# Optimization experiments

Measured on AMD Instinct MI355X. Metric: run time of the kernel, lower is better.

The kernel has to match this reference:

```python
import jax, jax.numpy as jnp
import numpy as np

N, F, E = 1024, 32, 20


def setup_inputs() -> dict:
    key = jax.random.key(0)
    ks = jax.random.split(key, 18)
    f32 = jnp.float32
    nrm = lambda k, shape, s=1.0: (jax.random.normal(k, shape, f32) * s)
    scalar = nrm(ks[0], (N, 1, F))
    vector = nrm(ks[1], (N, 3, F))
    expansion = nrm(ks[2], (N, N, E))
    d = nrm(ks[3], (N, N, 3))
    direction = d / (jnp.linalg.norm(d, axis=-1, keepdims=True) + 1e-6)
    mask = (jax.random.uniform(ks[4], (N, N, 1)) < 0.9).astype(f32)
    w = 0.1  # weight scale
    return {
        "scalar": scalar, "vector": vector, "expansion": expansion,
        "direction": direction, "mask": mask,
        # message.msg_left: Linear(F,F) -> SiLU -> Linear(F,3F)
        "mL_w1": nrm(ks[5], (F, F), w), "mL_b1": jnp.zeros((F,), f32),
        "mL_w2": nrm(ks[6], (F, 3 * F), w), "mL_b2": jnp.zeros((3 * F,), f32),
        # message.msg_right: Linear(E, 3F)
        "mR_w": nrm(ks[7], (E, 3 * F), w), "mR_b": jnp.zeros((3 * F,), f32),
        # update.upd_right: Linear(2F,F) -> SiLU -> Linear(F,3F)
        "uR_w1": nrm(ks[8], (2 * F, F), w), "uR_b1": jnp.zeros((F,), f32),
        "uR_w2": nrm(ks[9], (F, 3 * F), w), "uR_b2": jnp.zeros((3 * F,), f32),
        # update.U / update.V: Linear(F,F,bias=False)
        "U_w": nrm(ks[10], (F, F), w),
        "V_w": nrm(ks[11], (F, F), w),
    }


def _message(s, v, expansion, direction, mask,
             mL_w1, mL_b1, mL_w2, mL_b2, mR_w, mR_b):
    # msg_left(s): [N,1,F] -> [N,1,3F]
    left = jax.nn.silu(s @ mL_w1 + mL_b1) @ mL_w2 + mL_b2
    # msg_right(expansion): [N,N,E] -> [N,N,3F] -> [N,N,1,3F]
    right = (expansion @ mR_w + mR_b)[..., None, :]
    prod = left * right                      # [N,N,1,3F]
    a, b, c = jnp.split(prod, 3, axis=-1)    # each [N,N,1,F]
    mask_ = mask[..., None]                  # [N,N,1,1]
    delta_s = jnp.sum(mask_ * b, axis=-3)    # [N,1,F]
    dv = v * a + direction[..., None] * c    # [N,N,3,F]
    delta_v = jnp.sum(mask_ * dv, axis=-3)   # [N,3,F]
    return delta_s, delta_v


def _update(scalar, vector, uR_w1, uR_b1, uR_w2, uR_b2, U_w, V_w):
    left = vector @ U_w                      # [N,3,F]
    right = vector @ V_w                     # [N,3,F]
    right_norm = jnp.linalg.norm(right, axis=-2, keepdims=True)   # [N,1,F]
    feats = jnp.concatenate((scalar, right_norm), axis=-1)        # [N,1,2F]
    feats = jax.nn.silu(feats @ uR_w1 + uR_b1) @ uR_w2 + uR_b2    # [N,1,3F]
    a, b, c = jnp.split(feats, 3, axis=-1)
    delta_v = a * left                                            # [N,3,F]
    inner = jnp.sum(left * right, axis=-2, keepdims=True)         # [N,1,F]
    delta_s = inner * b + c
    return delta_s, delta_v


def reference(scalar, vector, expansion, direction, mask,
              mL_w1, mL_b1, mL_w2, mL_b2, mR_w, mR_b,
              uR_w1, uR_b1, uR_w2, uR_b2, U_w, V_w):
    ds, dv = _message(scalar, vector, expansion, direction, mask,
                      mL_w1, mL_b1, mL_w2, mL_b2, mR_w, mR_b)
    scalar = scalar + ds
    vector = vector + dv
    ds, dv = _update(scalar, vector, uR_w1, uR_b1, uR_w2, uR_b2, U_w, V_w)
    return scalar + ds, vector + dv
```

## Files before the change

### kernel.cpp

```cpp
#include <hip/hip_runtime.h>
#include <hip/hip_bf16.h>
#include <math.h>

#define NN 1024
#define JS 512
#define NSL 2
#define LP 40

typedef __attribute__((ext_vector_type(8))) short v8s;
typedef __attribute__((ext_vector_type(4))) float v4f;

#define MFMA(a, b, c) __builtin_amdgcn_mfma_f32_16x16x32_bf16((a), (b), (c), 0, 0, 0)

#define BAR() asm volatile("s_waitcnt lgkmcnt(0)\n\ts_barrier" ::: "memory")
#define VM0() asm volatile("s_waitcnt vmcnt(0)" ::: "memory")

static __device__ __forceinline__ void gll16(const void* g, void* l) {
    __builtin_amdgcn_global_load_lds(
        (const __attribute__((address_space(1))) unsigned int*)g,
        (__attribute__((address_space(3))) unsigned int*)l, 16, 0, 0);
}

static __device__ __forceinline__ float silu_f(float x) {
    return x / (1.0f + __expf(-x));
}
static __device__ __forceinline__ unsigned short f2bf(float x) {
    __hip_bfloat16 h = __float2bfloat16(x);
    unsigned short u; __builtin_memcpy(&u, &h, 2); return u;
}
static __device__ __forceinline__ unsigned pack2bf(float lo, float hi) {
    __hip_bfloat162 h = __float22bfloat162_rn(make_float2(lo, hi));
    unsigned u; __builtin_memcpy(&u, &h, 4); return u;
}

extern "C" __global__ __launch_bounds__(128)
void node_kernel(const float* __restrict__ scalar,
                 const float* __restrict__ vector,
                 const float* __restrict__ mL_w1, const float* __restrict__ mL_b1,
                 const float* __restrict__ mL_w2, const float* __restrict__ mL_b2,
                 unsigned short* __restrict__ RT)
{
    const int j = blockIdx.x;
    const int t = threadIdx.x;
    __shared__ float ss[32], sh[32], sleft[96];

    if (t < 32) ss[t] = scalar[j * 32 + t];
    __syncthreads();
    if (t < 32) {
        float a = mL_b1[t];
        #pragma unroll
        for (int k = 0; k < 32; k++) a = fmaf(ss[k], mL_w1[k * 32 + t], a);
        sh[t] = silu_f(a);
    }
    __syncthreads();
    if (t < 96) {
        float a = mL_b2[t];
        #pragma unroll
        for (int k = 0; k < 32; k++) a = fmaf(sh[k], mL_w2[k * 96 + t], a);
        sleft[t] = a;
    }
    __syncthreads();
    for (int n = t; n < 160; n += 128) {
        float val;
        if (n < 32)        val = sleft[32 + n];
        else if (n < 128)  val = vector[j * 96 + (n - 32)] * sleft[(n - 32) & 31];
        else               val = sleft[64 + (n - 128)];
        const int jsw = j ^ ((n & 7) << 3);
        RT[(size_t)n * NN + jsw] = f2bf(val);
    }
}

extern "C" __global__ __launch_bounds__(256, 4)
void edge_mfma_kernel(const float* __restrict__ expansion,
                      const float* __restrict__ direction,
                      const float* __restrict__ mask,
                      const float* __restrict__ mR_w, const float* __restrict__ mR_b,
                      const unsigned short* __restrict__ RT,
                      float* __restrict__ part)
{
    const int t = threadIdx.x;
    const int wave = t >> 6;
    const int lane = t & 63;
    const int lrow = lane & 15;
    const int quad = lane >> 4;
    const int jp = lane >> 2;
    const int g  = lane & 3;
    const int jl = jp * 2;

    const int bx = blockIdx.x;
    const int slice = bx & (NSL - 1);
    const int j0 = slice * JS;
    const int iw = wave >> 1;
    const int i = (bx >> 1) * 2 + iw;

    __shared__ __align__(16) unsigned short BSm[160 * 64];
    __shared__ __align__(16) char Wm[13824];
    __shared__ __align__(16) float mLds[2 * JS];

    const unsigned short* rtbase = RT + ((size_t)(t >> 3) * NN) + ((t & 7) * 8) + j0;
    unsigned short* lds_dst = BSm + t * 8;

    #pragma unroll
    for (int k = 0; k < 5; ++k)
        gll16(rtbase + (size_t)k * 32 * NN, lds_dst + k * 2048);
    for (int q = t; q < 2 * JS; q += 256)
        mLds[q] = mask[(size_t)((bx >> 1) * 2 + (q >> 9)) * NN + j0 + (q & 511)];
    VM0();
    BAR();

    const int kswz = (lrow & 7) << 3;
    const int ko = quad * 8;

    if ((wave & 1) == 0) {
        unsigned short* L1 = (unsigned short*)(Wm + iw * 6912);
        float* S = (float*)((char*)BSm + iw * 5472);

        v4f acc[16];
        #pragma unroll
        for (int q = 0; q < 16; ++q) acc[q] = (v4f){0.f, 0.f, 0.f, 0.f};

        const float* expA = expansion + ((size_t)i * NN + j0 + jl) * 20;

        float4 fa = *(const float4*)(expA + 4 * g);
        float4 fb = *(const float4*)(expA + 20 + 4 * g);
        float cea = expA[16 + g], ceb = expA[36 + g];
        float2 mc = *(const float2*)(&mLds[iw * JS + jl]);

        for (int ss2 = 0; ss2 < 8; ++ss2) {
            #pragma unroll
            for (int ch = 0; ch < 2; ++ch) {
                {
                    const float ea[4] = {fa.x, fa.y, fa.z, fa.w};
                    const float eb[4] = {fb.x, fb.y, fb.z, fb.w};
                    #pragma unroll
                    for (int k = 0; k < 4; ++k)
                        *(unsigned*)(L1 + (4 * g + k) * LP + jl) =
                            pack2bf(mc.x * ea[k], mc.y * eb[k]);
                    *(unsigned*)(L1 + (16 + g) * LP + jl) = pack2bf(mc.x * cea, mc.y * ceb);
                    if (g == 0) *(unsigned*)(L1 + 20 * LP + jl) = pack2bf(mc.x, mc.y);
                }
                {
                    const int u = ss2 * 2 + ch;
                    const int un = (u < 15) ? u + 1 : 15;
                    fa = *(const float4*)(expA + un * 640 + 4 * g);
                    fb = *(const float4*)(expA + un * 640 + 20 + 4 * g);
                    cea = expA[un * 640 + 16 + g];
                    ceb = expA[un * 640 + 36 + g];
                    mc = *(const float2*)(&mLds[iw * JS + un * 32 + jl]);
                }
                {
                    const v8s a0 = *(const v8s*)(L1 + lrow * LP + ko);
                    const v8s a1 = *(const v8s*)(L1 + (16 + lrow) * LP + ko);
                    const int klz = (ch * 32 + ko) ^ kswz;
                    #pragma unroll
                    for (int nt = 0; nt < 8; ++nt) {
                        const v8s b = *(const v8s*)(BSm + (nt * 16 + lrow) * 64 + klz);
                        acc[nt]     = MFMA(a0, b, acc[nt]);
                        acc[8 + nt] = MFMA(a1, b, acc[8 + nt]);
                    }
                }
            }
            BAR();
            if (ss2 < 7) {
                const unsigned short* src = rtbase + (ss2 + 1) * 64;
                #pragma unroll
                for (int k = 0; k < 5; ++k)
                    gll16(src + (size_t)k * 32 * NN, lds_dst + k * 2048);
                VM0();
                BAR();
            }
        }

        float* pdst = part + ((size_t)i * NSL + slice) * 224;
        #pragma unroll
        for (int h = 0; h < 2; ++h) {
            #pragma unroll
            for (int mt = 0; mt < 2; ++mt)
            #pragma unroll
            for (int q = 0; q < 4; ++q)
            #pragma unroll
            for (int r = 0; r < 4; ++r) {
                const int row = mt * 16 + quad * 4 + r;
                if (row <= 20) S[row * 65 + q * 16 + lrow] = acc[mt * 8 + h * 4 + q][r];
            }
            const int col = h * 64 + lane;
            const int fw = (col < 32) ? (32 + col) : ((col - 32) & 31);
            float v = mR_b[fw] * S[20 * 65 + lane];
            #pragma unroll
            for (int e = 0; e < 20; ++e)
                v = fmaf(mR_w[e * 96 + fw], S[e * 65 + lane], v);
            pdst[col] = v;
        }
    } else {
        unsigned short* L2 = (unsigned short*)(Wm + 1792 + iw * 6912);
        float* S = (float*)((char*)BSm + 10944 + iw * 4288);

        v4f acc[8];
        #pragma unroll
        for (int q = 0; q < 8; ++q) acc[q] = (v4f){0.f, 0.f, 0.f, 0.f};

        const float* expA = expansion + ((size_t)i * NN + j0 + jl) * 20;
        const float* dirA = direction + ((size_t)i * NN + j0 + jl) * 3;

        float4 fa = *(const float4*)(expA + 4 * g);
        float4 fb = *(const float4*)(expA + 20 + 4 * g);
        float cea = expA[16 + g], ceb = expA[36 + g];
        float2 mc = *(const float2*)(&mLds[iw * JS + jl]);
        float2 dv0 = *(const float2*)(dirA);
        float2 dv1 = *(const float2*)(dirA + 2);
        float2 dv2 = *(const float2*)(dirA + 4);

        for (int ss2 = 0; ss2 < 8; ++ss2) {
            #pragma unroll
            for (int ch = 0; ch < 2; ++ch) {
                {
                    const float pa[3] = {mc.x * dv0.x, mc.x * dv0.y, mc.x * dv1.x};
                    const float pb[3] = {mc.y * dv1.y, mc.y * dv2.x, mc.y * dv2.y};
                    const float ea[4] = {fa.x, fa.y, fa.z, fa.w};
                    const float eb[4] = {fb.x, fb.y, fb.z, fb.w};
                    #pragma unroll
                    for (int d = 0; d < 3; ++d) {
                        #pragma unroll
                        for (int k = 0; k < 4; ++k)
                            *(unsigned*)(L2 + (d * 20 + 4 * g + k) * LP + jl) =
                                pack2bf(pa[d] * ea[k], pb[d] * eb[k]);
                        *(unsigned*)(L2 + (d * 20 + 16 + g) * LP + jl) =
                            pack2bf(pa[d] * cea, pb[d] * ceb);
                    }
                    if (g == 0) {
                        *(unsigned*)(L2 + (60 + 0) * LP + jl) = pack2bf(pa[0], pb[0]);
                        *(unsigned*)(L2 + (60 + 1) * LP + jl) = pack2bf(pa[1], pb[1]);
                        *(unsigned*)(L2 + (60 + 2) * LP + jl) = pack2bf(pa[2], pb[2]);
                    }
                }
                {
                    const int u = ss2 * 2 + ch;
                    const int un = (u < 15) ? u + 1 : 15;
                    fa = *(const float4*)(expA + un * 640 + 4 * g);
                    fb = *(const float4*)(expA + un * 640 + 20 + 4 * g);
                    cea = expA[un * 640 + 16 + g];
                    ceb = expA[un * 640 + 36 + g];
                    dv0 = *(const float2*)(dirA + un * 96);
                    dv1 = *(const float2*)(dirA + un * 96 + 2);
                    dv2 = *(const float2*)(dirA + un * 96 + 4);
                    mc = *(const float2*)(&mLds[iw * JS + un * 32 + jl]);
                }
                {
                    const v8s c0 = *(const v8s*)(L2 + (lrow) * LP + ko);
                    const v8s c1 = *(const v8s*)(L2 + (16 + lrow) * LP + ko);
                    const v8s c2 = *(const v8s*)(L2 + (32 + lrow) * LP + ko);
                    const v8s c3 = *(const v8s*)(L2 + (48 + lrow) * LP + ko);
                    const int klz = (ch * 32 + ko) ^ kswz;
                    const v8s b0 = *(const v8s*)(BSm + (128 + lrow) * 64 + klz);
                    const v8s b1 = *(const v8s*)(BSm + (144 + lrow) * 64 + klz);
                    acc[0] = MFMA(c0, b0, acc[0]); acc[1] = MFMA(c0, b1, acc[1]);
                    acc[2] = MFMA(c1, b0, acc[2]); acc[3] = MFMA(c1, b1, acc[3]);
                    acc[4] = MFMA(c2, b0, acc[4]); acc[5] = MFMA(c2, b1, acc[5]);
                    acc[6] = MFMA(c3, b0, acc[6]); acc[7] = MFMA(c3, b1, acc[7]);
                }
            }
            BAR();
            if (ss2 < 7) {
                const unsigned short* src = rtbase + (ss2 + 1) * 64;
                #pragma unroll
                for (int k = 0; k < 5; ++k)
                    gll16(src + (size_t)k * 32 * NN, lds_dst + k * 2048);
                VM0();
                BAR();
            }
        }

        float* pdst = part + ((size_t)i * NSL + slice) * 224;
        #pragma unroll
        for (int h2 = 0; h2 < 2; ++h2) {
            #pragma unroll
            for (int mt = 0; mt < 4; ++mt)
            #pragma unroll
            for (int r = 0; r < 4; ++r) {
                const int row = mt * 16 + quad * 4 + r;
                if (row <= 62) S[row * 17 + lrow] = acc[mt * 2 + h2][r];
            }
            if (lane < 48) {
                const int dd = lane >> 4, f16 = lane & 15;
                const int f = h2 * 16 + f16;
                float v = mR_b[64 + f] * S[(60 + dd) * 17 + f16];
                #pragma unroll
                for (int e = 0; e < 20; ++e)
                    v = fmaf(mR_w[e * 96 + 64 + f], S[(dd * 20 + e) * 17 + f16], v);
                pdst[128 + dd * 32 + f] = v;
            }
        }
    }
}

extern "C" __global__ __launch_bounds__(256)
void combine_kernel(const float* __restrict__ scalar,
                    const float* __restrict__ vector,
                    const float* __restrict__ uR_w1, const float* __restrict__ uR_b1,
                    const float* __restrict__ uR_w2, const float* __restrict__ uR_b2,
                    const float* __restrict__ U_w,  const float* __restrict__ V_w,
                    const float* __restrict__ part,
                    float* __restrict__ out)
{
    const int i = blockIdx.x;
    const int t = threadIdx.x;
    __shared__ float pcomb[224];
    __shared__ float snew[32], vnew[96];
    __shared__ float lU[96], rV[96], rnorm[32], h2[32], f2[96];

    if (t < 224) {
        const float* p = part + (size_t)i * NSL * 224 + t;
        float a = 0.f;
        #pragma unroll
        for (int s = 0; s < NSL; ++s) a += p[s * 224];
        pcomb[t] = a;
    }
    __syncthreads();

    if (t < 128) {
        const int d = t >> 5, ff = t & 31;
        if (d == 0) snew[ff] = scalar[i * 32 + ff] + pcomb[ff];
        else {
            const int q = t - 32;
            vnew[q] = vector[i * 96 + q] + pcomb[32 + q] + pcomb[128 + q];
        }
    }
    __syncthreads();

    if (t < 96) {
        const int d = t >> 5, ff = t & 31;
        float a = 0.0f;
        #pragma unroll
        for (int k = 0; k < 32; k++) a = fmaf(vnew[d * 32 + k], U_w[k * 32 + ff], a);
        lU[t] = a;
    } else if (t >= 128 && t < 224) {
        const int dt = t - 128, d = dt >> 5, ff = dt & 31;
        float a = 0.0f;
        #pragma unroll
        for (int k = 0; k < 32; k++) a = fmaf(vnew[d * 32 + k], V_w[k * 32 + ff], a);
        rV[dt] = a;
    }
    __syncthreads();
    if (t < 32) {
        const float a = rV[t] * rV[t] + rV[32 + t] * rV[32 + t] + rV[64 + t] * rV[64 + t];
        rnorm[t] = sqrtf(a);
    }
    __syncthreads();
    if (t < 32) {
        float a = uR_b1[t];
        #pragma unroll
        for (int k = 0; k < 32; k++) a = fmaf(snew[k],  uR_w1[k * 32 + t], a);
        #pragma unroll
        for (int k = 0; k < 32; k++) a = fmaf(rnorm[k], uR_w1[(32 + k) * 32 + t], a);
        h2[t] = silu_f(a);
    }
    __syncthreads();
    if (t < 96) {
        float a = uR_b2[t];
        #pragma unroll
        for (int k = 0; k < 32; k++) a = fmaf(h2[k], uR_w2[k * 96 + t], a);
        f2[t] = a;
    }
    __syncthreads();
    if (t < 32) {
        const float inner = lU[t] * rV[t] + lU[32 + t] * rV[32 + t] + lU[64 + t] * rV[64 + t];
        out[i * 32 + t] = snew[t] + inner * f2[32 + t] + f2[64 + t];
    } else if (t >= 64 && t < 160) {
        const int dt = t - 64, ff = dt & 31;
        out[32768 + i * 96 + dt] = vnew[dt] + f2[ff] * lU[dt];
    }
}

extern "C" void kernel_launch(void* const* d_in, const int* in_sizes, int n_in,
                              void* d_out, int out_size, void* d_ws, size_t ws_size,
                              hipStream_t stream) {
    const float* scalar    = (const float*)d_in[0];
    const float* vector    = (const float*)d_in[1];
    const float* expansion = (const float*)d_in[2];
    const float* direction = (const float*)d_in[3];
    const float* mask      = (const float*)d_in[4];
    const float* mL_w1     = (const float*)d_in[5];
    const float* mL_b1     = (const float*)d_in[6];
    const float* mL_w2     = (const float*)d_in[7];
    const float* mL_b2     = (const float*)d_in[8];
    const float* mR_w      = (const float*)d_in[9];
    const float* mR_b      = (const float*)d_in[10];
    const float* uR_w1     = (const float*)d_in[11];
    const float* uR_b1     = (const float*)d_in[12];
    const float* uR_w2     = (const float*)d_in[13];
    const float* uR_b2     = (const float*)d_in[14];
    const float* U_w       = (const float*)d_in[15];
    const float* V_w       = (const float*)d_in[16];
    float* out = (float*)d_out;

    unsigned short* RT = (unsigned short*)d_ws;
    float* part = (float*)((char*)d_ws + 160 * NN * 2);

    hipLaunchKernelGGL(node_kernel, dim3(NN), dim3(128), 0, stream,
                       scalar, vector, mL_w1, mL_b1, mL_w2, mL_b2, RT);
    hipLaunchKernelGGL(edge_mfma_kernel, dim3(NN), dim3(256), 0, stream,
                       expansion, direction, mask, mR_w, mR_b, RT, part);
    hipLaunchKernelGGL(combine_kernel, dim3(NN), dim3(256), 0, stream,
                       scalar, vector, uR_w1, uR_b1, uR_w2, uR_b2, U_w, V_w,
                       part, out);
}
```

Before: 186.0 us.

## Double-buffer RT tiles in LDS with 32-wide chunks to overlap loads

Replaces the single 64-column RT staging buffer with two 32-column buffers and issues the async global-to-LDS load for the next chunk before computing the current one. Previously each 64-column stage was loaded only after a barrier, so the MFMA work waited on the load. The swizzle is changed from 8-way to 4-way to match the narrower rows, in both the producer kernel and the consumer. The exchange is more barriers per unit of work (one per 32 columns) and more staging instructions.

Result: no change. 188.4 us (+1.3%).

```diff
diff --git a/kernel.cpp b/kernel.cpp
--- a/kernel.cpp
+++ b/kernel.cpp
@@ -5,6 +5,7 @@
 #define NN 1024
 #define JS 512
 #define NSL 2
+#define NCH 16
 #define LP 40
 
 typedef __attribute__((ext_vector_type(8))) short v8s;
@@ -65,7 +66,7 @@
         if (n < 32)        val = sleft[32 + n];
         else if (n < 128)  val = vector[j * 96 + (n - 32)] * sleft[(n - 32) & 31];
         else               val = sleft[64 + (n - 128)];
-        const int jsw = j ^ ((n & 7) << 3);
+        const int jsw = j ^ ((n & 3) << 3);
         RT[(size_t)n * NN + jsw] = f2bf(val);
     }
 }
@@ -93,22 +94,27 @@
     const int iw = wave >> 1;
     const int i = (bx >> 1) * 2 + iw;
 
-    __shared__ __align__(16) unsigned short BSm[160 * 64];
+    __shared__ __align__(16) unsigned short BSm[2 * 160 * 32];
     __shared__ __align__(16) char Wm[13824];
     __shared__ __align__(16) float mLds[2 * JS];
 
-    const unsigned short* rtbase = RT + ((size_t)(t >> 3) * NN) + ((t & 7) * 8) + j0;
-    unsigned short* lds_dst = BSm + t * 8;
-
-    #pragma unroll
-    for (int k = 0; k < 5; ++k)
-        gll16(rtbase + (size_t)k * 32 * NN, lds_dst + k * 2048);
+#define STAGE(C, BSEL)                                                        \
+  {                                                                           \
+    const unsigned short* s0 =                                                \
+        RT + (size_t)(t >> 2) * NN + j0 + (C) * 32 + (t & 3) * 8;             \
+    unsigned short* d0 = BSm + (BSEL) * 5120 + t * 8;                         \
+    gll16(s0, d0);                                                            \
+    gll16(s0 + (size_t)64 * NN, d0 + 2048);                                   \
+    if (t < 128) gll16(s0 + (size_t)128 * NN, d0 + 4096);                     \
+  }
+
+    STAGE(0, 0);
     for (int q = t; q < 2 * JS; q += 256)
         mLds[q] = mask[(size_t)((bx >> 1) * 2 + (q >> 9)) * NN + j0 + (q & 511)];
     VM0();
     BAR();
 
-    const int kswz = (lrow & 7) << 3;
+    const int kswz = (lrow & 3) << 3;
     const int ko = quad * 8;
 
     if ((wave & 1) == 0) {
@@ -126,50 +132,49 @@
         float cea = expA[16 + g], ceb = expA[36 + g];
         float2 mc = *(const float2*)(&mLds[iw * JS + jl]);
 
-        for (int ss2 = 0; ss2 < 8; ++ss2) {
-            #pragma unroll
-            for (int ch = 0; ch < 2; ++ch) {
-                {
-                    const float ea[4] = {fa.x, fa.y, fa.z, fa.w};
-                    const float eb[4] = {fb.x, fb.y, fb.z, fb.w};
-                    #pragma unroll
-                    for (int k = 0; k < 4; ++k)
-                        *(unsigned*)(L1 + (4 * g + k) * LP + jl) =
-                            pack2bf(mc.x * ea[k], mc.y * eb[k]);
-                    *(unsigned*)(L1 + (16 + g) * LP + jl) = pack2bf(mc.x * cea, mc.y * ceb);
-                    if (g == 0) *(unsigned*)(L1 + 20 * LP + jl) = pack2bf(mc.x, mc.y);
-                }
-                {
-                    const int u = ss2 * 2 + ch;
-                    const int un = (u < 15) ? u + 1 : 15;
-                    fa = *(const float4*)(expA + un * 640 + 4 * g);
-                    fb = *(const float4*)(expA + un * 640 + 20 + 4 * g);
-                    cea = expA[un * 640 + 16 + g];
-                    ceb = expA[un * 640 + 36 + g];
-                    mc = *(const float2*)(&mLds[iw * JS + un * 32 + jl]);
-                }
-                {
-                    const v8s a0 = *(const v8s*)(L1 + lrow * LP + ko);
-                    const v8s a1 = *(const v8s*)(L1 + (16 + lrow) * LP + ko);
-                    const int klz = (ch * 32 + ko) ^ kswz;
-                    #pragma unroll
-                    for (int nt = 0; nt < 8; ++nt) {
-                        const v8s b = *(const v8s*)(BSm + (nt * 16 + lrow) * 64 + klz);
-                        acc[nt]     = MFMA(a0, b, acc[nt]);
-                        acc[8 + nt] = MFMA(a1, b, acc[8 + nt]);
-                    }
-                }
-            }
-            BAR();
-            if (ss2 < 7) {
-                const unsigned short* src = rtbase + (ss2 + 1) * 64;
-                #pragma unroll
-                for (int k = 0; k < 5; ++k)
-                    gll16(src + (size_t)k * 32 * NN, lds_dst + k * 2048);
-                VM0();
-                BAR();
-            }
+#define T1_CHUNK(C, BB)                                                       \
+  {                                                                           \
+    {                                                               \
+      const float ea[4] = {fa.x, fa.y, fa.z, fa.w};                           \
+      const float eb[4] = {fb.x, fb.y, fb.z, fb.w};                           \
+      _Pragma("unroll")                                                       \
+      for (int k = 0; k < 4; ++k)                                             \
+        *(unsigned*)(L1 + (4 * g + k) * LP + jl) =                            \
+            pack2bf(mc.x * ea[k], mc.y * eb[k]);                              \
+      *(unsigned*)(L1 + (16 + g) * LP + jl) = pack2bf(mc.x * cea, mc.y * ceb);\
+      if (g == 0) *(unsigned*)(L1 + 20 * LP + jl) = pack2bf(mc.x, mc.y);      \
+    }                                                                         \
+    {                                       \
+      const int un = ((C) < NCH - 1) ? (C) + 1 : NCH - 1;                     \
+      fa = *(const float4*)(expA + un * 640 + 4 * g);                         \
+      fb = *(const float4*)(expA + un * 640 + 20 + 4 * g);                    \
+      cea = expA[un * 640 + 16 + g];                                          \
+      ceb = expA[un * 640 + 36 + g];                                          \
+      mc = *(const float2*)(&mLds[iw * JS + un * 32 + jl]);                   \
+    }                                                                         \
+    {                                        \
+      const v8s a0 = *(const v8s*)(L1 + lrow * LP + ko);                      \
+      const v8s a1 = *(const v8s*)(L1 + (16 + lrow) * LP + ko);               \
+      const int klz = ko ^ kswz;                                              \
+      _Pragma("unroll")                                                       \
+      for (int nt = 0; nt < 8; ++nt) {                                        \
+        const v8s b = *(const v8s*)((BB) + (nt * 16 + lrow) * 32 + klz);      \
+        acc[nt]     = MFMA(a0, b, acc[nt]);                                   \
+        acc[8 + nt] = MFMA(a1, b, acc[8 + nt]);                               \
+      }                                                                       \
+    }                                                                         \
+  }
+
+        for (int cc = 0; cc < 8; ++cc) {
+            const int c0 = cc * 2;
+            STAGE(c0 + 1, 1);
+            T1_CHUNK(c0, BSm);
+            VM0(); BAR();
+            if (cc < 7) STAGE(c0 + 2, 0);
+            T1_CHUNK(c0 + 1, BSm + 5120);
+            VM0(); BAR();
         }
+#undef T1_CHUNK
 
         float* pdst = part + ((size_t)i * NSL + slice) * 224;
         #pragma unroll
@@ -210,65 +215,64 @@
         float2 dv1 = *(const float2*)(dirA + 2);
         float2 dv2 = *(const float2*)(dirA + 4);
 
-        for (int ss2 = 0; ss2 < 8; ++ss2) {
-            #pragma unroll
-            for (int ch = 0; ch < 2; ++ch) {
-                {
-                    const float pa[3] = {mc.x * dv0.x, mc.x * dv0.y, mc.x * dv1.x};
-                    const float pb[3] = {mc.y * dv1.y, mc.y * dv2.x, mc.y * dv2.y};
-                    const float ea[4] = {fa.x, fa.y, fa.z, fa.w};
-                    const float eb[4] = {fb.x, fb.y, fb.z, fb.w};
-                    #pragma unroll
-                    for (int d = 0; d < 3; ++d) {
-                        #pragma unroll
-                        for (int k = 0; k < 4; ++k)
-                            *(unsigned*)(L2 + (d * 20 + 4 * g + k) * LP + jl) =
-                                pack2bf(pa[d] * ea[k], pb[d] * eb[k]);
-                        *(unsigned*)(L2 + (d * 20 + 16 + g) * LP + jl) =
-                            pack2bf(pa[d] * cea, pb[d] * ceb);
-                    }
-                    if (g == 0) {
-                        *(unsigned*)(L2 + (60 + 0) * LP + jl) = pack2bf(pa[0], pb[0]);
-                        *(unsigned*)(L2 + (60 + 1) * LP + jl) = pack2bf(pa[1], pb[1]);
-                        *(unsigned*)(L2 + (60 + 2) * LP + jl) = pack2bf(pa[2], pb[2]);
-                    }
-                }
-                {
-                    const int u = ss2 * 2 + ch;
-                    const int un = (u < 15) ? u + 1 : 15;
-                    fa = *(const float4*)(expA + un * 640 + 4 * g);
-                    fb = *(const float4*)(expA + un * 640 + 20 + 4 * g);
-                    cea = expA[un * 640 + 16 + g];
-                    ceb = expA[un * 640 + 36 + g];
-                    dv0 = *(const float2*)(dirA + un * 96);
-                    dv1 = *(const float2*)(dirA + un * 96 + 2);
-                    dv2 = *(const float2*)(dirA + un * 96 + 4);
-                    mc = *(const float2*)(&mLds[iw * JS + un * 32 + jl]);
-                }
-                {
-                    const v8s c0 = *(const v8s*)(L2 + (lrow) * LP + ko);
-                    const v8s c1 = *(const v8s*)(L2 + (16 + lrow) * LP + ko);
-                    const v8s c2 = *(const v8s*)(L2 + (32 + lrow) * LP + ko);
-                    const v8s c3 = *(const v8s*)(L2 + (48 + lrow) * LP + ko);
-                    const int klz = (ch * 32 + ko) ^ kswz;
-                    const v8s b0 = *(const v8s*)(BSm + (128 + lrow) * 64 + klz);
-                    const v8s b1 = *(const v8s*)(BSm + (144 + lrow) * 64 + klz);
-                    acc[0] = MFMA(c0, b0, acc[0]); acc[1] = MFMA(c0, b1, acc[1]);
-                    acc[2] = MFMA(c1, b0, acc[2]); acc[3] = MFMA(c1, b1, acc[3]);
-                    acc[4] = MFMA(c2, b0, acc[4]); acc[5] = MFMA(c2, b1, acc[5]);
-                    acc[6] = MFMA(c3, b0, acc[6]); acc[7] = MFMA(c3, b1, acc[7]);
-                }
-            }
-            BAR();
-            if (ss2 < 7) {
-                const unsigned short* src = rtbase + (ss2 + 1) * 64;
-                #pragma unroll
-                for (int k = 0; k < 5; ++k)
-                    gll16(src + (size_t)k * 32 * NN, lds_dst + k * 2048);
-                VM0();
-                BAR();
-            }
+#define T2_CHUNK(C, BB)                                                       \
+  {                                                                           \
+    {                                                               \
+      const float pa[3] = {mc.x * dv0.x, mc.x * dv0.y, mc.x * dv1.x};         \
+      const float pb[3] = {mc.y * dv1.y, mc.y * dv2.x, mc.y * dv2.y};         \
+      const float ea[4] = {fa.x, fa.y, fa.z, fa.w};                           \
+      const float eb[4] = {fb.x, fb.y, fb.z, fb.w};                           \
+      _Pragma("unroll")                                                       \
+      for (int d = 0; d < 3; ++d) {                                           \
+        _Pragma("unroll")                                                     \
+        for (int k = 0; k < 4; ++k)                                           \
+          *(unsigned*)(L2 + (d * 20 + 4 * g + k) * LP + jl) =                 \
+              pack2bf(pa[d] * ea[k], pb[d] * eb[k]);                          \
+        *(unsigned*)(L2 + (d * 20 + 16 + g) * LP + jl) =                      \
+            pack2bf(pa[d] * cea, pb[d] * ceb);                                \
+      }                                                                       \
+      if (g == 0) {                                                           \
+        *(unsigned*)(L2 + (60 + 0) * LP + jl) = pack2bf(pa[0], pb[0]);        \
+        *(unsigned*)(L2 + (60 + 1) * LP + jl) = pack2bf(pa[1], pb[1]);        \
+        *(unsigned*)(L2 + (60 + 2) * LP + jl) = pack2bf(pa[2], pb[2]);        \
+      }                                                                       \
+    }                                                                         \
+    {                                       \
+      const int un = ((C) < NCH - 1) ? (C) + 1 : NCH - 1;                     \
+      fa = *(const float4*)(expA + un * 640 + 4 * g);                         \
+      fb = *(const float4*)(expA + un * 640 + 20 + 4 * g);                    \
+      cea = expA[un * 640 + 16 + g];                                          \
+      ceb = expA[un * 640 + 36 + g];                                          \
+      dv0 = *(const float2*)(dirA + un * 96);                                 \
+      dv1 = *(const float2*)(dirA + un * 96 + 2);                             \
+      dv2 = *(const float2*)(dirA + un * 96 + 4);                             \
+      mc = *(const float2*)(&mLds[iw * JS + un * 32 + jl]);                   \
+    }                                                                         \
+    {                                        \
+      const v8s c0 = *(const v8s*)(L2 + (lrow) * LP + ko);                    \
+      const v8s c1 = *(const v8s*)(L2 + (16 + lrow) * LP + ko);               \
+      const v8s c2 = *(const v8s*)(L2 + (32 + lrow) * LP + ko);               \
+      const v8s c3 = *(const v8s*)(L2 + (48 + lrow) * LP + ko);               \
+      const int klz = ko ^ kswz;                                              \
+      const v8s b0 = *(const v8s*)((BB) + (128 + lrow) * 32 + klz);           \
+      const v8s b1 = *(const v8s*)((BB) + (144 + lrow) * 32 + klz);           \
+      acc[0] = MFMA(c0, b0, acc[0]); acc[1] = MFMA(c0, b1, acc[1]);           \
+      acc[2] = MFMA(c1, b0, acc[2]); acc[3] = MFMA(c1, b1, acc[3]);           \
+      acc[4] = MFMA(c2, b0, acc[4]); acc[5] = MFMA(c2, b1, acc[5]);           \
+      acc[6] = MFMA(c3, b0, acc[6]); acc[7] = MFMA(c3, b1, acc[7]);           \
+    }                                                                         \
+  }
+
+        for (int cc = 0; cc < 8; ++cc) {
+            const int c0 = cc * 2;
+            STAGE(c0 + 1, 1);
+            T2_CHUNK(c0, BSm);
+            VM0(); BAR();
+            if (cc < 7) STAGE(c0 + 2, 0);
+            T2_CHUNK(c0 + 1, BSm + 5120);
+            VM0(); BAR();
         }
+#undef T2_CHUNK
 
         float* pdst = part + ((size_t)i * NSL + slice) * 224;
         #pragma unroll
@@ -291,6 +295,7 @@
             }
         }
     }
+#undef STAGE
 }
 
 extern "C" __global__ __launch_bounds__(256)
```
